# Performance work log

Hardware: AMD Instinct MI355X
Metric: run time of the kernel (lower is better)

The kernel has to match this reference:

```python
import jax, jax.numpy as jnp
import numpy as np

B, S, D = 1, 2048, 1024          # batch, seq, n_embd
E, F = 16, 1024                  # n_routed_experts, moe_intermediate_size
NG, TKG, K = 4, 2, 4             # n_group, topk_group, num_experts_per_tok
NSH = 2                          # n_shared_experts
SCALE = 2.5                      # routed_scaling_factor
STD = 0.02
EPG = E // NG                    # experts per group


def setup_inputs() -> dict:
    key = jax.random.key(0)
    ks = jax.random.split(key, 8)
    return {
        "hidden_states": jax.random.normal(ks[0], (B, S, D), jnp.float32),
        "router_w": jax.random.normal(ks[1], (E, D), jnp.float32) * STD,   # gate.weight
        "bias": jnp.zeros((E,), jnp.float32),                              # e_score_correction_bias
        "gate_w": jax.random.normal(ks[2], (E, D, F), jnp.float32) * STD,  # per-expert gate_proj (transposed)
        "up_w": jax.random.normal(ks[3], (E, D, F), jnp.float32) * STD,    # per-expert up_proj
        "down_w": jax.random.normal(ks[4], (E, F, D), jnp.float32) * STD,  # per-expert down_proj
        "sh_gate_w": jax.random.normal(ks[5], (D, NSH * F), jnp.float32) * STD,
        "sh_up_w": jax.random.normal(ks[6], (D, NSH * F), jnp.float32) * STD,
        "sh_down_w": jax.random.normal(ks[7], (NSH * F, D), jnp.float32) * STD,
    }


def _route(x_flat, router_w, bias):
    # x_flat: [T, D] -> topk_idx [T, K], topk_w [T, K]
    logits = x_flat.astype(jnp.float32) @ router_w.T          # [T, E]
    scores = jax.nn.sigmoid(logits)
    s = scores + bias[None, :]                                # scores_for_choice
    sg = s.reshape(-1, NG, EPG)
    group_score = jax.lax.top_k(sg, 2)[0].sum(-1)             # sum of top-2 per group [T, NG]
    gidx = jax.lax.top_k(group_score, TKG)[1]                 # [T, TKG]
    gmask = jnp.sum(jax.nn.one_hot(gidx, NG, dtype=jnp.float32), axis=1) > 0   # [T, NG]
    emask = jnp.repeat(gmask, EPG, axis=1)                    # [T, E]
    masked = jnp.where(emask, s, -1.0)
    topk_idx = jax.lax.top_k(masked, K)[1]                    # [T, K]
    tw = jnp.take_along_axis(scores, topk_idx, axis=1)        # gather raw sigmoid scores
    tw = tw / (tw.sum(-1, keepdims=True) + 1e-20)             # norm_topk_prob
    tw = tw * SCALE
    return topk_idx, tw


def reference(hidden_states, router_w, bias, gate_w, up_w, down_w,
              sh_gate_w, sh_up_w, sh_down_w):
    x = hidden_states.reshape(-1, D)                          # [T, D]
    topk_idx, tw = _route(x, router_w, bias)
    # combine weights per (token, expert): scatter-add of topk weights
    combine = (jax.nn.one_hot(topk_idx, E, dtype=tw.dtype) * tw[..., None]).sum(1)  # [T, E]
    # per-expert SwiGLU MLPs (dense dispatch, masked combine == index_add semantics)
    h = jnp.einsum('td,edf->etf', x, gate_w)                  # [E, T, F]
    u = jnp.einsum('td,edf->etf', x, up_w)
    y = jnp.einsum('etf,efd->etd', jax.nn.silu(h) * u, down_w)  # [E, T, D]
    routed = jnp.einsum('etd,te->td', y, combine)             # weighted combine
    # shared experts
    sh = (jax.nn.silu(x @ sh_gate_w) * (x @ sh_up_w)) @ sh_down_w
    return (routed + sh).reshape(hidden_states.shape)
```

## Files before the change

### kernel.cpp

```cpp
#include <hip/hip_runtime.h>
#include <cstdint>
#include <cstddef>


#define T_TOK 2048
#define DIM   1024
#define NEXP  16
#define MAXTILES 80
#define SH_TILES 32
#define GRID_Y (MAXTILES + SH_TILES)
#define NBLK (8 * GRID_Y)
#define ABASE_SH 10240

typedef __bf16 bf16x8_t __attribute__((ext_vector_type(8)));
typedef float  f32x4_t  __attribute__((ext_vector_type(4)));
typedef unsigned short ushort8_t __attribute__((ext_vector_type(8)));
typedef unsigned short ushort4_t __attribute__((ext_vector_type(4)));

#define OFF_XB     (0UL)
#define OFF_SHGT   (4UL<<20)
#define OFF_SHUT   (8UL<<20)
#define OFF_GATET  (12UL<<20)
#define OFF_UPT    (44UL<<20)
#define OFF_DOWNT  (76UL<<20)
#define OFF_SHDT   (108UL<<20)
#define OFF_ACT    (112UL<<20)
#define OFF_YSLOT  (140UL<<20)
#define OFF_PART   (0UL)
#define OFF_CTRL   (160UL<<20)
#define CT_OFFSETS  128
#define CT_NTILES   192
#define CT_TILEEXP  256
#define CT_SLOTTOK  4096
#define CT_TKSLOT   49152
#define CT_TOPKIDX  81920
#define CT_TOPKW    114688

__device__ __forceinline__ unsigned short f2bf(float f) {
  __bf16 h = (__bf16)f;
  return __builtin_bit_cast(unsigned short, h);
}
__device__ __forceinline__ float bf2f(unsigned short u) {
  unsigned int v = ((unsigned int)u) << 16;
  return __builtin_bit_cast(float, v);
}
__device__ __forceinline__ void gld16(const void* g, void* l) {
  __builtin_amdgcn_global_load_lds(
      (const __attribute__((address_space(1))) void*)(g),
      (__attribute__((address_space(3))) void*)(l), 16, 0, 0);
}

#define VWAIT6 asm volatile("s_waitcnt vmcnt(6)" ::: "memory")
#define VWAIT4 asm volatile("s_waitcnt vmcnt(4)" ::: "memory")
#define VWAIT0 asm volatile("s_waitcnt vmcnt(0)" ::: "memory")
#define BAR { __builtin_amdgcn_s_barrier(); __builtin_amdgcn_sched_barrier(0); }

__device__ __forceinline__ void tbody(const float* __restrict__ src,
                                      unsigned short* __restrict__ dst,
                                      int R, int C) {
  __shared__ unsigned short tile[2][64 * 68];
  int cT = blockIdx.x * 64, rT = blockIdx.y * 128;
  int t = threadIdx.x;
  int rb = t >> 4, cb = t & 15;
  float f[2][4][4];
#pragma unroll
  for (int s = 0; s < 2; s++)
#pragma unroll
    for (int i = 0; i < 4; i++) {
      float4 v = *(const float4*)(src + (long)(rT + s * 64 + 4 * rb + i) * C + cT + 4 * cb);
      f[s][i][0] = v.x; f[s][i][1] = v.y; f[s][i][2] = v.z; f[s][i][3] = v.w;
    }
#pragma unroll
  for (int s = 0; s < 2; s++)
#pragma unroll
    for (int j = 0; j < 4; j++) {
      ushort4_t o;
      o[0] = f2bf(f[s][0][j]); o[1] = f2bf(f[s][1][j]);
      o[2] = f2bf(f[s][2][j]); o[3] = f2bf(f[s][3][j]);
      int c = 4 * cb + j;
      *(ushort4_t*)&tile[s][c * 68 + 4 * rb] = o;
    }
  __syncthreads();
#pragma unroll
  for (int s = 0; s < 2; s++)
#pragma unroll
    for (int p = 0; p < 2; p++) {
      int q = t + 256 * p;
      int c = q >> 3, r0 = (q & 7) * 8;
      ushort4_t lo = *(const ushort4_t*)&tile[s][c * 68 + r0];
      ushort4_t hi = *(const ushort4_t*)&tile[s][c * 68 + r0 + 4];
      ushort8_t w8 = {lo[0], lo[1], lo[2], lo[3], hi[0], hi[1], hi[2], hi[3]};
      *(ushort8_t*)(dst + (long)(cT + c) * R + rT + s * 64 + r0) = w8;
    }
}

__global__ void k_transpose(const float* __restrict__ src, unsigned short* __restrict__ dst,
                            int R, int C) {
  long b = blockIdx.z;
  tbody(src + b * (long)R * C, dst + b * (long)R * C, R, C);
}

__global__ void k_transpose3(const float* __restrict__ g, const float* __restrict__ u,
                             const float* __restrict__ d, unsigned short* __restrict__ gT,
                             unsigned short* __restrict__ uT, unsigned short* __restrict__ dT) {
  int z = blockIdx.z;
  int which = z >> 4;
  long b = z & 15;
  const float* s = (which == 0) ? g : (which == 1) ? u : d;
  unsigned short* t = (which == 0) ? gT : (which == 1) ? uT : dT;
  tbody(s + b * 1048576L, t + b * 1048576L, 1024, 1024);
}

__global__ void k_transpose_sh(const float* __restrict__ sg, const float* __restrict__ su,
                               unsigned short* __restrict__ gT, unsigned short* __restrict__ uT) {
  const float* s = blockIdx.z ? su : sg;
  unsigned short* t = blockIdx.z ? uT : gT;
  tbody(s, t, 1024, 2048);
}

__global__ __launch_bounds__(256) void k_router(
    const float* __restrict__ x, const float* __restrict__ rw,
    const float* __restrict__ bias, int* __restrict__ topk_idx,
    float* __restrict__ topk_w, unsigned short* __restrict__ xb) {
  int t = blockIdx.x, tid = threadIdx.x;
  int wv = tid >> 6, lane = tid & 63;
  float4 xv = ((const float4*)(x + (size_t)t * DIM))[tid];
  ushort4_t xo;
  xo[0] = f2bf(xv.x); xo[1] = f2bf(xv.y); xo[2] = f2bf(xv.z); xo[3] = f2bf(xv.w);
  ((ushort4_t*)(xb + (size_t)t * DIM))[tid] = xo;
  float part[NEXP];
#pragma unroll
  for (int e = 0; e < NEXP; e++) {
    float4 wr = ((const float4*)(rw + (size_t)e * DIM))[tid];
    part[e] = xv.x * wr.x + xv.y * wr.y + xv.z * wr.z + xv.w * wr.w;
  }
  __shared__ float wsum_s[4 * NEXP];
#pragma unroll
  for (int e = 0; e < NEXP; e++) {
    float v = part[e];
#pragma unroll
    for (int off = 32; off; off >>= 1) v += __shfl_xor(v, off, 64);
    if (lane == 0) wsum_s[wv * NEXP + e] = v;
  }
  __syncthreads();
  if (tid == 0) {
    float r_sc[NEXP], r_s[NEXP];
#pragma unroll
    for (int e = 0; e < NEXP; e++) {
      float logit = wsum_s[e] + wsum_s[NEXP + e] + wsum_s[2 * NEXP + e] +
                    wsum_s[3 * NEXP + e];
      float sc = 1.f / (1.f + expf(-logit));
      r_sc[e] = sc;
      r_s[e] = sc + bias[e];
    }
    float gs[4];
#pragma unroll
    for (int g = 0; g < 4; g++) {
      float m1 = -1e30f, m2 = -1e30f;
#pragma unroll
      for (int j = 0; j < 4; j++) {
        float v = r_s[g * 4 + j];
        if (v > m1) { m2 = m1; m1 = v; } else if (v > m2) m2 = v;
      }
      gs[g] = m1 + m2;
    }
    int g1 = 0;
    for (int g = 1; g < 4; g++) if (gs[g] > gs[g1]) g1 = g;
    int g2 = -1;
    for (int g = 0; g < 4; g++) { if (g == g1) continue; if (g2 < 0 || gs[g] > gs[g2]) g2 = g; }
    int taken = 0, idx[4];
    float w[4], wsum = 1e-20f;
#pragma unroll
    for (int k = 0; k < 4; k++) {
      float best = -1e30f; int bi = 0;
#pragma unroll
      for (int e2 = 0; e2 < 16; e2++) {
        if (taken & (1 << e2)) continue;
        int g = e2 >> 2;
        float v = (g == g1 || g == g2) ? r_s[e2] : -1.f;
        if (v > best) { best = v; bi = e2; }
      }
      taken |= 1 << bi; idx[k] = bi;
    }
#pragma unroll
    for (int k = 0; k < 4; k++) { w[k] = r_sc[idx[k]]; wsum += w[k]; }
    float sc2 = 2.5f / wsum;
#pragma unroll
    for (int k = 0; k < 4; k++) {
      topk_idx[t * 4 + k] = idx[k];
      topk_w[t * 4 + k] = w[k] * sc2;
    }
  }
}

__global__ __launch_bounds__(256) void k_route_post(
    const int* __restrict__ topk_idx, int* __restrict__ offsets,
    int* __restrict__ tile_expert, int* __restrict__ n_tiles,
    int* __restrict__ slot_token, int* __restrict__ tk_slot) {
  __shared__ int cnt[NEXP][257];
  __shared__ int offs[NEXP], tot[NEXP];
  int tid = threadIdx.x;
  int4 ent[8];
#pragma unroll
  for (int i = 0; i < 8; i++) ent[i] = ((const int4*)topk_idx)[tid * 8 + i];
  int lc[NEXP];
#pragma unroll
  for (int j = 0; j < NEXP; j++) lc[j] = 0;
#pragma unroll
  for (int i = 0; i < 8; i++) {
    int es[4] = {ent[i].x, ent[i].y, ent[i].z, ent[i].w};
#pragma unroll
    for (int k = 0; k < 4; k++)
#pragma unroll
      for (int j = 0; j < NEXP; j++) lc[j] += (es[k] == j) ? 1 : 0;
  }
#pragma unroll
  for (int j = 0; j < NEXP; j++) cnt[j][tid] = lc[j];
  __syncthreads();
  if (tid < NEXP) {
    int base = 0;
    for (int c = 0; c < 256; c += 8) {
      int v[8];
#pragma unroll
      for (int i = 0; i < 8; i++) v[i] = cnt[tid][c + i];
#pragma unroll
      for (int i = 0; i < 8; i++) { cnt[tid][c + i] = base; base += v[i]; }
    }
    tot[tid] = base;
  }
  __syncthreads();
  if (tid == 0) {
    int cum = 0, tt = 0;
    for (int e = 0; e < NEXP; e++) {
      offs[e] = cum;
      offsets[e] = cum;
      int nt = (tot[e] + 127) >> 7;
      for (int i = 0; i < nt; i++) tile_expert[tt++] = e;
      cum += nt << 7;
    }
    n_tiles[0] = tt;
  }
  __syncthreads();
  for (int e = 0; e < NEXP; e++) {
    int s0 = offs[e] + tot[e];
    int s1 = offs[e] + (((tot[e] + 127) >> 7) << 7);
    for (int s = s0 + tid; s < s1; s += 256) slot_token[s] = -1;
  }
  int lcur[NEXP];
#pragma unroll
  for (int j = 0; j < NEXP; j++) lcur[j] = offs[j] + cnt[j][tid];
#pragma unroll
  for (int i = 0; i < 8; i++) {
    int t = tid * 8 + i;
    int es[4] = {ent[i].x, ent[i].y, ent[i].z, ent[i].w};
#pragma unroll
    for (int k = 0; k < 4; k++) {
      int e = es[k], pos = 0;
#pragma unroll
      for (int j = 0; j < NEXP; j++) pos += (e == j) ? lcur[j] : 0;
#pragma unroll
      for (int j = 0; j < NEXP; j++) lcur[j] += (e == j) ? 1 : 0;
      slot_token[pos] = t;
      tk_slot[t * 4 + k] = pos;
    }
  }
}

__global__ __launch_bounds__(256, 2) void k_gateup(
    const unsigned short* __restrict__ xb, const unsigned short* __restrict__ gateT,
    const unsigned short* __restrict__ upT, const unsigned short* __restrict__ shGT,
    const unsigned short* __restrict__ shUT, unsigned short* __restrict__ act,
    const int* __restrict__ slot_token, const int* __restrict__ tile_expert,
    const int* __restrict__ n_tiles) {
  int o = blockIdx.x;
  int wk = (o & 7) * GRID_Y + (o >> 3);
  int nx = wk & 7, bt = wk >> 3;
  int NT = n_tiles[0];
  bool routed = bt < NT;
  const unsigned short *Bg, *Bu;
  int actbase, tokbase = 0;
  if (routed) {
    int e = tile_expert[bt];
    Bg = gateT + ((size_t)e << 20);
    Bu = upT + ((size_t)e << 20);
    actbase = bt * 128;
  } else {
    int st = bt - NT;
    if (st >= SH_TILES) return;
    int se = st >> 4, tt = st & 15;
    Bg = shGT + ((size_t)se << 20);
    Bu = shUT + ((size_t)se << 20);
    actbase = ABASE_SH + se * T_TOK + tt * 128;
    tokbase = tt * 128;
  }
  int n0 = nx * 128;

  __shared__ unsigned short lds[2 * 3 * 128 * 32];

  int tid = threadIdx.x;
  int w = tid >> 6, L = tid & 63;
  int c0 = w * 128 + L, c1 = c0 + 64;
  int ar0 = c0 >> 2, ar1 = c1 >> 2;
  int ch0 = (c0 & 3) ^ (ar0 & 3), ch1 = (c1 & 3) ^ (ar1 & 3);
  long arow0, arow1;
  if (routed) {
    int t0 = slot_token[bt * 128 + ar0]; if (t0 < 0) t0 = 0;
    int t1 = slot_token[bt * 128 + ar1]; if (t1 < 0) t1 = 0;
    arow0 = t0; arow1 = t1;
  } else {
    arow0 = tokbase + ar0; arow1 = tokbase + ar1;
  }
  const char* aA = (const char*)(xb + arow0 * 1024) + ch0 * 16;
  const char* aB = (const char*)(xb + arow1 * 1024) + ch1 * 16;
  const char* gA = (const char*)(Bg + (size_t)(n0 + ar0) * 1024) + ch0 * 16;
  const char* gB = (const char*)(Bg + (size_t)(n0 + ar1) * 1024) + ch1 * 16;
  const char* uA = (const char*)(Bu + (size_t)(n0 + ar0) * 1024) + ch0 * 16;
  const char* uB = (const char*)(Bu + (size_t)(n0 + ar1) * 1024) + ch1 * 16;
  const int a0o = w * 2048, a1o = w * 2048 + 1024;
  const int g0o = 8192 + w * 2048, g1o = 8192 + w * 2048 + 1024;
  const int u0o = 16384 + w * 2048, u1o = 16384 + w * 2048 + 1024;

  f32x4_t accg[4][4], accu[4][4];
#pragma unroll
  for (int i = 0; i < 4; i++)
#pragma unroll
    for (int j = 0; j < 4; j++) {
      accg[i][j] = f32x4_t{0.f, 0.f, 0.f, 0.f};
      accu[i][j] = f32x4_t{0.f, 0.f, 0.f, 0.f};
    }

  int mb = (w >> 1) * 64, nb = (w & 1) * 64;
  int lr = L & 15, quad = L >> 4;
  int sw = ((quad ^ (lr & 3)) << 3);

#define GU_STAGE(BOFF)                                                       \
  { char* bp = (char*)lds + (BOFF);                                          \
    gld16(aA, bp + a0o); gld16(aB, bp + a1o);                                \
    gld16(gA, bp + g0o); gld16(gB, bp + g1o);                                \
    gld16(uA, bp + u0o); gld16(uB, bp + u1o);                                \
    aA += 64; aB += 64; gA += 64; gB += 64; uA += 64; uB += 64; }

#define GU_COMPUTE(UOFF)                                                     \
  { const unsigned short* pA = lds + (UOFF);                                 \
    const unsigned short* pG = pA + 4096;                                    \
    const unsigned short* pU = pA + 8192;                                    \
    bf16x8_t af[4], bg[4], bu[4];                                            \
    _Pragma("unroll")                                                        \
    for (int i = 0; i < 4; i++) af[i] = *(const bf16x8_t*)(pA + (mb + 16 * i + lr) * 32 + sw); \
    _Pragma("unroll")                                                        \
    for (int i = 0; i < 4; i++) bg[i] = *(const bf16x8_t*)(pG + (nb + 16 * i + lr) * 32 + sw); \
    _Pragma("unroll")                                                        \
    for (int i = 0; i < 4; i++) bu[i] = *(const bf16x8_t*)(pU + (nb + 16 * i + lr) * 32 + sw); \
    _Pragma("unroll")                                                        \
    for (int i = 0; i < 4; i++)                                              \
      _Pragma("unroll")                                                      \
      for (int j = 0; j < 4; j++) {                                          \
        accg[i][j] = __builtin_amdgcn_mfma_f32_16x16x32_bf16(af[i], bg[j], accg[i][j], 0, 0, 0); \
        accu[i][j] = __builtin_amdgcn_mfma_f32_16x16x32_bf16(af[i], bu[j], accu[i][j], 0, 0, 0); \
      } }

  GU_STAGE(0); GU_STAGE(24576);
#pragma unroll 1
  for (int p = 0; p < 15; ++p) {
    VWAIT6; BAR; GU_COMPUTE(0);     BAR; GU_STAGE(0);
    VWAIT6; BAR; GU_COMPUTE(12288); BAR; GU_STAGE(24576);
  }
  VWAIT6; BAR; GU_COMPUTE(0);
  VWAIT0; BAR; GU_COMPUTE(12288);
#undef GU_STAGE
#undef GU_COMPUTE

#pragma unroll
  for (int i = 0; i < 4; i++) {
    int rowb = actbase + mb + 16 * i + quad * 4;
#pragma unroll
    for (int j = 0; j < 4; j++) {
      int col = n0 + nb + 16 * j + lr;
#pragma unroll
      for (int r = 0; r < 4; r++) {
        float h = accg[i][j][r];
        float u = accu[i][j][r];
        float a = h / (1.f + __expf(-h)) * u;
        act[(size_t)(rowb + r) * 1024 + col] = f2bf(a);
      }
    }
  }
}

__global__ __launch_bounds__(256, 2) void k_down(
    const unsigned short* __restrict__ act, const unsigned short* __restrict__ downT,
    const unsigned short* __restrict__ shDT, unsigned short* __restrict__ yslot,
    float* __restrict__ part, const int* __restrict__ tile_expert,
    const int* __restrict__ n_tiles) {
  int o = blockIdx.x;
  int wk = (o & 7) * GRID_Y + (o >> 3);
  int nx = wk & 7, bt = wk >> 3;
  int NT = n_tiles[0];
  bool routed = bt < NT;
  const unsigned short* B;
  size_t bstride;
  int abase, obase, se = 0;
  if (routed) {
    int e = tile_expert[bt];
    B = downT + ((size_t)e << 20);
    bstride = 1024;
    abase = bt * 128;
    obase = bt * 128;
  } else {
    int st = bt - NT;
    if (st >= SH_TILES) return;
    se = st >> 4;
    int tt = st & 15;
    B = shDT + se * 1024;
    bstride = 2048;
    abase = ABASE_SH + se * T_TOK + tt * 128;
    obase = tt * 128;
  }
  int n0 = nx * 128;

  __shared__ unsigned short lds[2 * 2 * 128 * 32];

  int tid = threadIdx.x;
  int w = tid >> 6, L = tid & 63;
  int c0 = w * 128 + L, c1 = c0 + 64;
  int ar0 = c0 >> 2, ar1 = c1 >> 2;
  int ch0 = (c0 & 3) ^ (ar0 & 3), ch1 = (c1 & 3) ^ (ar1 & 3);
  const char* aA = (const char*)(act + (size_t)(abase + ar0) * 1024) + ch0 * 16;
  const char* aB = (const char*)(act + (size_t)(abase + ar1) * 1024) + ch1 * 16;
  const char* bA = (const char*)(B + (size_t)(n0 + ar0) * bstride) + ch0 * 16;
  const char* bB = (const char*)(B + (size_t)(n0 + ar1) * bstride) + ch1 * 16;
  const int a0o = w * 2048, a1o = w * 2048 + 1024;
  const int b0o = 8192 + w * 2048, b1o = 8192 + w * 2048 + 1024;

  f32x4_t acc[4][4];
#pragma unroll
  for (int i = 0; i < 4; i++)
#pragma unroll
    for (int j = 0; j < 4; j++) acc[i][j] = f32x4_t{0.f, 0.f, 0.f, 0.f};

  int mb = (w >> 1) * 64, nb = (w & 1) * 64;
  int lr = L & 15, quad = L >> 4;
  int sw = ((quad ^ (lr & 3)) << 3);

#define DN_STAGE(BOFF)                                                       \
  { char* bp = (char*)lds + (BOFF);                                          \
    gld16(aA, bp + a0o); gld16(aB, bp + a1o);                                \
    gld16(bA, bp + b0o); gld16(bB, bp + b1o);                                \
    aA += 64; aB += 64; bA += 64; bB += 64; }

#define DN_COMPUTE(UOFF)                                                     \
  { const unsigned short* pA = lds + (UOFF);                                 \
    const unsigned short* pB = pA + 4096;                                    \
    bf16x8_t af[4], bb[4];                                                   \
    _Pragma("unroll")                                                        \
    for (int i = 0; i < 4; i++) af[i] = *(const bf16x8_t*)(pA + (mb + 16 * i + lr) * 32 + sw); \
    _Pragma("unroll")                                                        \
    for (int i = 0; i < 4; i++) bb[i] = *(const bf16x8_t*)(pB + (nb + 16 * i + lr) * 32 + sw); \
    _Pragma("unroll")                                                        \
    for (int i = 0; i < 4; i++)                                              \
      _Pragma("unroll")                                                      \
      for (int j = 0; j < 4; j++)                                            \
        acc[i][j] = __builtin_amdgcn_mfma_f32_16x16x32_bf16(af[i], bb[j], acc[i][j], 0, 0, 0); }

  DN_STAGE(0); DN_STAGE(16384);
#pragma unroll 1
  for (int p = 0; p < 15; ++p) {
    VWAIT4; BAR; DN_COMPUTE(0);    BAR; DN_STAGE(0);
    VWAIT4; BAR; DN_COMPUTE(8192); BAR; DN_STAGE(16384);
  }
  VWAIT4; BAR; DN_COMPUTE(0);
  VWAIT0; BAR; DN_COMPUTE(8192);
#undef DN_STAGE
#undef DN_COMPUTE

#pragma unroll
  for (int i = 0; i < 4; i++) {
    int rowb = obase + mb + 16 * i + quad * 4;
#pragma unroll
    for (int j = 0; j < 4; j++) {
      int col = n0 + nb + 16 * j + lr;
#pragma unroll
      for (int r = 0; r < 4; r++) {
        float v = acc[i][j][r];
        if (routed) yslot[(size_t)(rowb + r) * 1024 + col] = f2bf(v);
        else part[(size_t)se * (T_TOK * 1024) + (size_t)(rowb + r) * 1024 + col] = v;
      }
    }
  }
}

__global__ void k_gather(float* __restrict__ out, const float* __restrict__ partial,
                         const unsigned short* __restrict__ yslot,
                         const int* __restrict__ tk_slot, const float* __restrict__ topk_w) {
  int t = blockIdx.x, tid = threadIdx.x;
  int4 sl = ((const int4*)tk_slot)[t];
  float4 wv = ((const float4*)topk_w)[t];
  int d = 4 * tid;
  float4 p0 = *(const float4*)(partial + (size_t)t * 1024 + d);
  float4 p1 = *(const float4*)(partial + (size_t)(T_TOK * 1024) + (size_t)t * 1024 + d);
  float4 o = {p0.x + p1.x, p0.y + p1.y, p0.z + p1.z, p0.w + p1.w};
  const int s[4] = {sl.x, sl.y, sl.z, sl.w};
  const float wk[4] = {wv.x, wv.y, wv.z, wv.w};
#pragma unroll
  for (int k = 0; k < 4; k++) {
    ushort4_t y = *(const ushort4_t*)(yslot + (size_t)s[k] * 1024 + d);
    o.x += wk[k] * bf2f(y[0]);
    o.y += wk[k] * bf2f(y[1]);
    o.z += wk[k] * bf2f(y[2]);
    o.w += wk[k] * bf2f(y[3]);
  }
  *(float4*)(out + (size_t)t * 1024 + d) = o;
}

extern "C" void kernel_launch(void* const* d_in, const int* in_sizes, int n_in,
                              void* d_out, int out_size, void* d_ws, size_t ws_size,
                              hipStream_t stream) {
  const float* x = (const float*)d_in[0];
  const float* rw = (const float*)d_in[1];
  const float* bias = (const float*)d_in[2];
  const float* gw = (const float*)d_in[3];
  const float* uw = (const float*)d_in[4];
  const float* dw = (const float*)d_in[5];
  const float* sg = (const float*)d_in[6];
  const float* su = (const float*)d_in[7];
  const float* sd = (const float*)d_in[8];
  float* out = (float*)d_out;
  char* ws = (char*)d_ws;

  unsigned short* xb    = (unsigned short*)(ws + OFF_XB);
  unsigned short* shGT  = (unsigned short*)(ws + OFF_SHGT);
  unsigned short* shUT  = (unsigned short*)(ws + OFF_SHUT);
  unsigned short* gateT = (unsigned short*)(ws + OFF_GATET);
  unsigned short* upT   = (unsigned short*)(ws + OFF_UPT);
  unsigned short* downT = (unsigned short*)(ws + OFF_DOWNT);
  unsigned short* shDT  = (unsigned short*)(ws + OFF_SHDT);
  unsigned short* act   = (unsigned short*)(ws + OFF_ACT);
  unsigned short* yslot = (unsigned short*)(ws + OFF_YSLOT);
  float*          part  = (float*)(ws + OFF_PART);
  char* ctrl = ws + OFF_CTRL;
  int* offsets_    = (int*)(ctrl + CT_OFFSETS);
  int* n_tiles     = (int*)(ctrl + CT_NTILES);
  int* tile_expert = (int*)(ctrl + CT_TILEEXP);
  int* slot_token  = (int*)(ctrl + CT_SLOTTOK);
  int* tk_slot     = (int*)(ctrl + CT_TKSLOT);
  int* topk_idx    = (int*)(ctrl + CT_TOPKIDX);
  float* topk_w    = (float*)(ctrl + CT_TOPKW);

  k_transpose3<<<dim3(16, 8, 48), 256, 0, stream>>>(gw, uw, dw, gateT, upT, downT);
  k_transpose_sh<<<dim3(32, 8, 2), 256, 0, stream>>>(sg, su, shGT, shUT);
  k_transpose<<<dim3(16, 16, 1), 256, 0, stream>>>(sd, shDT, 2048, 1024);
  k_router<<<2048, 256, 0, stream>>>(x, rw, bias, topk_idx, topk_w, xb);
  k_route_post<<<1, 256, 0, stream>>>(topk_idx, offsets_, tile_expert, n_tiles,
                                      slot_token, tk_slot);
  k_gateup<<<NBLK, 256, 0, stream>>>(xb, gateT, upT, shGT, shUT, act,
                                     slot_token, tile_expert, n_tiles);
  k_down<<<NBLK, 256, 0, stream>>>(act, downT, shDT, yslot, part,
                                   tile_expert, n_tiles);
  k_gather<<<2048, 256, 0, stream>>>(out, part, yslot, tk_slot, topk_w);
}
```

Measured before the change: 420.7 us.

## Triple-buffer GEMM LDS pipelines and widen weight-transpose tiles to 128x128

The gate/up and down GEMM kernels move from double to triple LDS buffering. Each k-step now issues the next global-to-LDS stage right after a single barrier and before the MFMA compute, instead of barrier, compute, barrier, stage. This removes one barrier per step and overlaps loads with compute, at the cost of 50% more LDS per block, which may lower occupancy. The fp32-to-bf16 weight transpose kernels also switch to 128x128 tiles with half the grid in x, so each block does more work and issues wider stores.

```diff
diff --git a/kernel.cpp b/kernel.cpp
--- a/kernel.cpp
+++ b/kernel.cpp
@@ -58,40 +58,37 @@
 __device__ __forceinline__ void tbody(const float* __restrict__ src,
                                       unsigned short* __restrict__ dst,
                                       int R, int C) {
-  __shared__ unsigned short tile[2][64 * 68];
-  int cT = blockIdx.x * 64, rT = blockIdx.y * 128;
+  __shared__ unsigned short tile[128 * 132];
+  int cT = blockIdx.x * 128, rT = blockIdx.y * 128;
   int t = threadIdx.x;
-  int rb = t >> 4, cb = t & 15;
-  float f[2][4][4];
-#pragma unroll
-  for (int s = 0; s < 2; s++)
+  int rb = t >> 5, cb = t & 31;
+  float f[4][4][4];
+#pragma unroll
+  for (int p = 0; p < 4; p++)
 #pragma unroll
     for (int i = 0; i < 4; i++) {
-      float4 v = *(const float4*)(src + (long)(rT + s * 64 + 4 * rb + i) * C + cT + 4 * cb);
-      f[s][i][0] = v.x; f[s][i][1] = v.y; f[s][i][2] = v.z; f[s][i][3] = v.w;
-    }
-#pragma unroll
-  for (int s = 0; s < 2; s++)
+      float4 v = *(const float4*)(src + (long)(rT + p * 32 + 4 * rb + i) * C + cT + 4 * cb);
+      f[p][i][0] = v.x; f[p][i][1] = v.y; f[p][i][2] = v.z; f[p][i][3] = v.w;
+    }
+#pragma unroll
+  for (int p = 0; p < 4; p++)
 #pragma unroll
     for (int j = 0; j < 4; j++) {
       ushort4_t o;
-      o[0] = f2bf(f[s][0][j]); o[1] = f2bf(f[s][1][j]);
-      o[2] = f2bf(f[s][2][j]); o[3] = f2bf(f[s][3][j]);
-      int c = 4 * cb + j;
-      *(ushort4_t*)&tile[s][c * 68 + 4 * rb] = o;
+      o[0] = f2bf(f[p][0][j]); o[1] = f2bf(f[p][1][j]);
+      o[2] = f2bf(f[p][2][j]); o[3] = f2bf(f[p][3][j]);
+      *(ushort4_t*)&tile[(4 * cb + j) * 132 + p * 32 + 4 * rb] = o;
     }
   __syncthreads();
 #pragma unroll
-  for (int s = 0; s < 2; s++)
-#pragma unroll
-    for (int p = 0; p < 2; p++) {
-      int q = t + 256 * p;
-      int c = q >> 3, r0 = (q & 7) * 8;
-      ushort4_t lo = *(const ushort4_t*)&tile[s][c * 68 + r0];
-      ushort4_t hi = *(const ushort4_t*)&tile[s][c * 68 + r0 + 4];
-      ushort8_t w8 = {lo[0], lo[1], lo[2], lo[3], hi[0], hi[1], hi[2], hi[3]};
-      *(ushort8_t*)(dst + (long)(cT + c) * R + rT + s * 64 + r0) = w8;
-    }
+  for (int m = 0; m < 8; m++) {
+    int q = t + 256 * m;
+    int c = q >> 4, r0 = (q & 15) * 8;
+    ushort4_t lo = *(const ushort4_t*)&tile[c * 132 + r0];
+    ushort4_t hi = *(const ushort4_t*)&tile[c * 132 + r0 + 4];
+    ushort8_t w8 = {lo[0], lo[1], lo[2], lo[3], hi[0], hi[1], hi[2], hi[3]};
+    *(ushort8_t*)(dst + (long)(cT + c) * R + rT + r0) = w8;
+  }
 }
 
 __global__ void k_transpose(const float* __restrict__ src, unsigned short* __restrict__ dst,
@@ -295,7 +292,7 @@
   }
   int n0 = nx * 128;
 
-  __shared__ unsigned short lds[2 * 3 * 128 * 32];
+  __shared__ unsigned short lds[3 * 3 * 128 * 32];
 
   int tid = threadIdx.x;
   int w = tid >> 6, L = tid & 63;
@@ -361,9 +358,10 @@
 
   GU_STAGE(0); GU_STAGE(24576);
 #pragma unroll 1
-  for (int p = 0; p < 15; ++p) {
-    VWAIT6; BAR; GU_COMPUTE(0);     BAR; GU_STAGE(0);
-    VWAIT6; BAR; GU_COMPUTE(12288); BAR; GU_STAGE(24576);
+  for (int p = 0; p < 10; ++p) {
+    VWAIT6; BAR; GU_STAGE(49152); GU_COMPUTE(0);
+    VWAIT6; BAR; GU_STAGE(0);     GU_COMPUTE(12288);
+    VWAIT6; BAR; GU_STAGE(24576); GU_COMPUTE(24576);
   }
   VWAIT6; BAR; GU_COMPUTE(0);
   VWAIT0; BAR; GU_COMPUTE(12288);
@@ -418,7 +416,7 @@
   }
   int n0 = nx * 128;
 
-  __shared__ unsigned short lds[2 * 2 * 128 * 32];
+  __shared__ unsigned short lds[3 * 2 * 128 * 32];
 
   int tid = threadIdx.x;
   int w = tid >> 6, L = tid & 63;
@@ -464,9 +462,10 @@
 
   DN_STAGE(0); DN_STAGE(16384);
 #pragma unroll 1
-  for (int p = 0; p < 15; ++p) {
-    VWAIT4; BAR; DN_COMPUTE(0);    BAR; DN_STAGE(0);
-    VWAIT4; BAR; DN_COMPUTE(8192); BAR; DN_STAGE(16384);
+  for (int p = 0; p < 10; ++p) {
+    VWAIT4; BAR; DN_STAGE(32768); DN_COMPUTE(0);
+    VWAIT4; BAR; DN_STAGE(0);     DN_COMPUTE(8192);
+    VWAIT4; BAR; DN_STAGE(16384); DN_COMPUTE(16384);
   }
   VWAIT4; BAR; DN_COMPUTE(0);
   VWAIT0; BAR; DN_COMPUTE(8192);
@@ -546,9 +545,9 @@
   int* topk_idx    = (int*)(ctrl + CT_TOPKIDX);
   float* topk_w    = (float*)(ctrl + CT_TOPKW);
 
-  k_transpose3<<<dim3(16, 8, 48), 256, 0, stream>>>(gw, uw, dw, gateT, upT, downT);
-  k_transpose_sh<<<dim3(32, 8, 2), 256, 0, stream>>>(sg, su, shGT, shUT);
-  k_transpose<<<dim3(16, 16, 1), 256, 0, stream>>>(sd, shDT, 2048, 1024);
+  k_transpose3<<<dim3(8, 8, 48), 256, 0, stream>>>(gw, uw, dw, gateT, upT, downT);
+  k_transpose_sh<<<dim3(16, 8, 2), 256, 0, stream>>>(sg, su, shGT, shUT);
+  k_transpose<<<dim3(8, 16, 1), 256, 0, stream>>>(sd, shDT, 2048, 1024);
   k_router<<<2048, 256, 0, stream>>>(x, rw, bias, topk_idx, topk_w, xb);
   k_route_post<<<1, 256, 0, stream>>>(topk_idx, offsets_, tile_expert, n_tiles,
                                       slot_token, tk_slot);
```

After: 418.8 us. About the same (-0.4%).
